# Optimization experiments

Hardware: AMD Instinct MI355X
Metric: run time of the kernel (lower is better)

The kernel has to match this reference:

```python
import jax, jax.numpy as jnp
import numpy as np

OUT_C, IN_C, K = 64, 64, 3
H, W = 32, 32


def setup_inputs() -> dict:
    key = jax.random.key(0)
    k1, k2, k3 = jax.random.split(key, 3)
    x = jax.random.normal(k1, (1, H, W, IN_C), dtype=jnp.float32)
    # One rational activation (P5/Q4, PAU 'version A') per (out_c, in_c, ky, kx)
    w_num = jax.random.normal(k2, (OUT_C, IN_C, K, K, 6), dtype=jnp.float32) * 0.1
    w_den = jax.random.normal(k3, (OUT_C, IN_C, K, K, 4), dtype=jnp.float32) * 0.1
    return {"x": x, "w_num": w_num, "w_den": w_den}


def reference(x, w_num, w_den):
    # x: [1, H, W, C] -- original module only supports batch=1 (squeeze semantics)
    h, w, c = x.shape[1], x.shape[2], x.shape[3]
    pad = (K - 1) // 2
    xp = jnp.pad(x[0], ((pad, pad), (pad, pad), (0, 0)))  # [H+2p, W+2p, C]
    # patches[a,b,i,j,c] = xp[i+a, j+b, c]  (same 'same-padding' sliding window)
    patches = jnp.stack(
        [jnp.stack([xp[a:a + h, b:b + w, :] for b in range(K)], axis=0)
         for a in range(K)], axis=0)  # [K,K,H,W,C]
    # powers x^0..x^5, computed once and reused by numerator and denominator
    pows = jnp.stack([patches ** n for n in range(6)], axis=0)  # [6,K,K,H,W,C]
    # per (f,c,a,b) rational: P(x) = sum_n a_n x^n,  Q(x) = 1 + |sum_{n=1..4} b_n x^n|
    P = jnp.einsum('nabijc,fcabn->fabijc', pows, w_num)
    Q = 1.0 + jnp.abs(jnp.einsum('nabijc,fcabn->fabijc', pows[1:5], w_den))
    # sum contributions over kernel positions (a,b) and input channels c
    return jnp.sum(P / Q, axis=(1, 2, 5))  # [OUT_C, H, W]
```

## Files before the change

kernel.cpp:

```cpp
#include <hip/hip_runtime.h>
#include <math.h>

#define NOUT 64
#define NIN  64
#define HH   32
#define WW   32

#define NREC      (NOUT * 9 * NIN)
#define WPK_ELEMS (NREC * 12)
#define WN_WORDS  (NOUT * NIN * 9 * 6)
#define WD_WORDS  (NOUT * NIN * 9 * 4)

__global__ __launch_bounds__(256) void wpack_kernel(const float* __restrict__ wn,
                                                    const float* __restrict__ wd,
                                                    float* __restrict__ wpk) {
    int idx = blockIdx.x * 256 + threadIdx.x;
    if (idx < WN_WORDS) {
        int n  = idx % 6;
        int t  = idx / 6;
        int ab = t % 9;
        int t2 = t / 9;
        int c  = t2 & 63;
        int f  = t2 >> 6;
        wpk[((f * 9 + ab) * 64 + c) * 12 + n] = wn[idx];
    } else {
        int id2 = idx - WN_WORDS;
        int n  = id2 & 3;
        int t  = id2 >> 2;
        int ab = t % 9;
        int t2 = t / 9;
        int c  = t2 & 63;
        int f  = t2 >> 6;
        wpk[((f * 9 + ab) * 64 + c) * 12 + 6 + n] = wd[id2];
    }
}

__global__ __launch_bounds__(512, 8) void kan_main(const float* __restrict__ x,
                                                   const float* __restrict__ wpk,
                                                   float* __restrict__ out) {
    __shared__ float xt[4 * 34 * 64];

    int bid  = blockIdx.x;
    int wgid = (bid & 7) * 128 + (bid >> 3);
    int f    = wgid >> 4;
    int band = wgid & 15;
    int i0   = band * 2;

    int tid  = threadIdx.x;
    int lane = tid & 63;
    int wave = tid >> 6;

#pragma unroll
    for (int k = 0; k < 17; ++k) {
        int idx = k * 512 + tid;
        int c   = idx & 63;
        int pos = idx >> 6;
        int col = pos % 34;
        int t   = pos / 34;
        int gi  = i0 - 1 + t;
        int gj  = col - 1;
        float v = 0.0f;
        if (gi >= 0 && gi < HH && gj >= 0 && gj < WW)
            v = x[(gi * WW + gj) * NIN + c];
        xt[idx] = v;
    }
    __syncthreads();

    int wr = wave >> 2;
    int j0 = (wave & 3) * 8;
    int i  = i0 + wr;

    float acc[8];
#pragma unroll
    for (int p = 0; p < 8; ++p) acc[p] = 0.0f;

    const float4* w4 = (const float4*)(wpk + ((size_t)(f * 9) * 64 + lane) * 12);

#pragma unroll 2
    for (int ab = 0; ab < 9; ++ab) {
        const int a = ab / 3, b = ab % 3;
        float4 wA = w4[ab * 192 + 0];
        float4 wB = w4[ab * 192 + 1];
        float4 wC = w4[ab * 192 + 2];

        const float* xb = &xt[((wr + a) * 34 + (j0 + b)) * 64 + lane];
#pragma unroll
        for (int p = 0; p < 8; ++p) {
            float xv = xb[p * 64];
            float pn = fmaf(wB.y, xv, wB.x);
            pn = fmaf(pn, xv, wA.w);
            pn = fmaf(pn, xv, wA.z);
            pn = fmaf(pn, xv, wA.y);
            pn = fmaf(pn, xv, wA.x);
            float qn = fmaf(wC.y, xv, wC.x);
            qn = fmaf(qn, xv, wB.w);
            qn = fmaf(qn, xv, wB.z);
            float den = 1.0f + fabsf(xv * qn);
            acc[p] = fmaf(pn, __builtin_amdgcn_rcpf(den), acc[p]);
        }
    }

#pragma unroll
    for (int p = 0; p < 8; ++p) {
        float s = acc[p];
        s += __shfl_xor(s, 32, 64);
        s += __shfl_xor(s, 16, 64);
        s += __shfl_xor(s, 8, 64);
        s += __shfl_xor(s, 4, 64);
        s += __shfl_xor(s, 2, 64);
        s += __shfl_xor(s, 1, 64);
        if (lane == p) out[f * (HH * WW) + i * WW + j0 + p] = s;
    }
}

__global__ __launch_bounds__(256) void kan_fallback(const float* __restrict__ x,
                                                    const float* __restrict__ wn,
                                                    const float* __restrict__ wd,
                                                    float* __restrict__ out) {
    __shared__ float red[256];
    int bid = blockIdx.x;
    int t = bid & 15;
    int f = bid >> 4;
    int tid = threadIdx.x;
    int g = tid >> 6;
    int p = tid & 63;
    int r = p >> 5;
    int j = p & 31;
    int i = t * 2 + r;
    int c0 = g * 16;
    const float* wnb = wn + (f * NIN + c0) * 9 * 6;
    const float* wdb = wd + (f * NIN + c0) * 9 * 4;
    float acc = 0.0f;
    for (int c = 0; c < 16; ++c) {
        float xv[9];
#pragma unroll
        for (int a = 0; a < 3; ++a)
#pragma unroll
            for (int b = 0; b < 3; ++b) {
                int ii = i + a - 1, jj = j + b - 1;
                bool inb = (ii >= 0) && (ii < HH) && (jj >= 0) && (jj < WW);
                xv[a * 3 + b] = inb ? x[(ii * WW + jj) * NIN + (c0 + c)] : 0.0f;
            }
        const float* wnc = wnb + c * 54;
        const float* wdc = wdb + c * 36;
#pragma unroll
        for (int ab = 0; ab < 9; ++ab) {
            float xx = xv[ab];
            float pn = fmaf(wnc[ab * 6 + 5], xx, wnc[ab * 6 + 4]);
            pn = fmaf(pn, xx, wnc[ab * 6 + 3]);
            pn = fmaf(pn, xx, wnc[ab * 6 + 2]);
            pn = fmaf(pn, xx, wnc[ab * 6 + 1]);
            pn = fmaf(pn, xx, wnc[ab * 6 + 0]);
            float qn = fmaf(wdc[ab * 4 + 3], xx, wdc[ab * 4 + 2]);
            qn = fmaf(qn, xx, wdc[ab * 4 + 1]);
            qn = fmaf(qn, xx, wdc[ab * 4 + 0]);
            float den = 1.0f + fabsf(xx * qn);
            acc = fmaf(pn, __builtin_amdgcn_rcpf(den), acc);
        }
    }
    red[tid] = acc;
    __syncthreads();
    if (tid < 64) {
        float s = red[tid] + red[tid + 64] + red[tid + 128] + red[tid + 192];
        int rr = tid >> 5;
        int jj = tid & 31;
        out[f * (HH * WW) + (t * 2 + rr) * WW + jj] = s;
    }
}

extern "C" void kernel_launch(void* const* d_in, const int* in_sizes, int n_in,
                              void* d_out, int out_size, void* d_ws, size_t ws_size,
                              hipStream_t stream) {
    const float* x  = (const float*)d_in[0];
    const float* wn = (const float*)d_in[1];
    const float* wd = (const float*)d_in[2];
    float* out = (float*)d_out;

    const size_t need = (size_t)WPK_ELEMS * sizeof(float);

    if (ws_size >= need) {
        float* wpk = (float*)d_ws;
        const int pack_total = WN_WORDS + WD_WORDS;
        wpack_kernel<<<pack_total / 256, 256, 0, stream>>>(wn, wd, wpk);
        kan_main<<<1024, 512, 0, stream>>>(x, wpk, out);
    } else {
        kan_fallback<<<NOUT * 16, 256, 0, stream>>>(x, wn, wd, out);
    }
}
```

Before: 28.08 us.

## Drop weight-pack kernel and remap threads to pixels with wave-uniform scalar weights

Removes the separate weight repacking launch and reads the original weight tensors directly. Each wave now owns 8 input channels and each lane one output pixel, so the weights are uniform across the wave (readfirstlane) and can be fetched with scalar loads. The input tile is transposed into a channel-major shared layout with an odd stride to avoid bank conflicts. The cross-lane shuffle reduction is replaced by an 8-way shared-memory reduction over waves. This saves one launch and the per-lane vector weight loads, at the cost of strided global-to-shared writes and a block barrier for the final reduction.

```diff
diff --git a/kernel.cpp b/kernel.cpp
--- a/kernel.cpp
+++ b/kernel.cpp
@@ -5,40 +5,14 @@
 #define NIN  64
 #define HH   32
 #define WW   32
-
-#define NREC      (NOUT * 9 * NIN)
-#define WPK_ELEMS (NREC * 12)
-#define WN_WORDS  (NOUT * NIN * 9 * 6)
-#define WD_WORDS  (NOUT * NIN * 9 * 4)
-
-__global__ __launch_bounds__(256) void wpack_kernel(const float* __restrict__ wn,
-                                                    const float* __restrict__ wd,
-                                                    float* __restrict__ wpk) {
-    int idx = blockIdx.x * 256 + threadIdx.x;
-    if (idx < WN_WORDS) {
-        int n  = idx % 6;
-        int t  = idx / 6;
-        int ab = t % 9;
-        int t2 = t / 9;
-        int c  = t2 & 63;
-        int f  = t2 >> 6;
-        wpk[((f * 9 + ab) * 64 + c) * 12 + n] = wn[idx];
-    } else {
-        int id2 = idx - WN_WORDS;
-        int n  = id2 & 3;
-        int t  = id2 >> 2;
-        int ab = t % 9;
-        int t2 = t / 9;
-        int c  = t2 & 63;
-        int f  = t2 >> 6;
-        wpk[((f * 9 + ab) * 64 + c) * 12 + 6 + n] = wd[id2];
-    }
-}
+#define XSTR 137
 
 __global__ __launch_bounds__(512, 8) void kan_main(const float* __restrict__ x,
-                                                   const float* __restrict__ wpk,
+                                                   const float* __restrict__ wn,
+                                                   const float* __restrict__ wd,
                                                    float* __restrict__ out) {
-    __shared__ float xt[4 * 34 * 64];
+    __shared__ float xt[NIN * XSTR];
+    __shared__ float red[512];
 
     int bid  = blockIdx.x;
     int wgid = (bid & 7) * 128 + (bid >> 3);
@@ -46,125 +20,66 @@
     int band = wgid & 15;
     int i0   = band * 2;
 
-    int tid  = threadIdx.x;
-    int lane = tid & 63;
-    int wave = tid >> 6;
+    int tid = threadIdx.x;
 
 #pragma unroll
     for (int k = 0; k < 17; ++k) {
         int idx = k * 512 + tid;
         int c   = idx & 63;
         int pos = idx >> 6;
+        int t   = pos / 34;
         int col = pos % 34;
-        int t   = pos / 34;
         int gi  = i0 - 1 + t;
         int gj  = col - 1;
         float v = 0.0f;
         if (gi >= 0 && gi < HH && gj >= 0 && gj < WW)
             v = x[(gi * WW + gj) * NIN + c];
-        xt[idx] = v;
+        xt[c * XSTR + pos] = v;
     }
     __syncthreads();
 
-    int wr = wave >> 2;
-    int j0 = (wave & 3) * 8;
-    int i  = i0 + wr;
+    int lane = tid & 63;
+    int wv   = __builtin_amdgcn_readfirstlane(tid >> 6);
+    int r    = lane >> 5;
+    int j    = lane & 31;
 
-    float acc[8];
+    float acc = 0.0f;
+
+    const float* wnf = wn + (size_t)(f * NIN + wv * 8) * 54;
+    const float* wdf = wd + (size_t)(f * NIN + wv * 8) * 36;
+
+    for (int cc = 0; cc < 8; ++cc) {
+        const float* wnc = wnf + cc * 54;
+        const float* wdc = wdf + cc * 36;
+        const float* xc  = &xt[(wv * 8 + cc) * XSTR + r * 34 + j];
 #pragma unroll
-    for (int p = 0; p < 8; ++p) acc[p] = 0.0f;
-
-    const float4* w4 = (const float4*)(wpk + ((size_t)(f * 9) * 64 + lane) * 12);
-
-#pragma unroll 2
-    for (int ab = 0; ab < 9; ++ab) {
-        const int a = ab / 3, b = ab % 3;
-        float4 wA = w4[ab * 192 + 0];
-        float4 wB = w4[ab * 192 + 1];
-        float4 wC = w4[ab * 192 + 2];
-
-        const float* xb = &xt[((wr + a) * 34 + (j0 + b)) * 64 + lane];
+        for (int a = 0; a < 3; ++a) {
 #pragma unroll
-        for (int p = 0; p < 8; ++p) {
-            float xv = xb[p * 64];
-            float pn = fmaf(wB.y, xv, wB.x);
-            pn = fmaf(pn, xv, wA.w);
-            pn = fmaf(pn, xv, wA.z);
-            pn = fmaf(pn, xv, wA.y);
-            pn = fmaf(pn, xv, wA.x);
-            float qn = fmaf(wC.y, xv, wC.x);
-            qn = fmaf(qn, xv, wB.w);
-            qn = fmaf(qn, xv, wB.z);
-            float den = 1.0f + fabsf(xv * qn);
-            acc[p] = fmaf(pn, __builtin_amdgcn_rcpf(den), acc[p]);
+            for (int b = 0; b < 3; ++b) {
+                const int ab = a * 3 + b;
+                float xv = xc[a * 34 + b];
+                float pn = fmaf(wnc[ab * 6 + 5], xv, wnc[ab * 6 + 4]);
+                pn = fmaf(pn, xv, wnc[ab * 6 + 3]);
+                pn = fmaf(pn, xv, wnc[ab * 6 + 2]);
+                pn = fmaf(pn, xv, wnc[ab * 6 + 1]);
+                pn = fmaf(pn, xv, wnc[ab * 6 + 0]);
+                float qn = fmaf(wdc[ab * 4 + 3], xv, wdc[ab * 4 + 2]);
+                qn = fmaf(qn, xv, wdc[ab * 4 + 1]);
+                qn = fmaf(qn, xv, wdc[ab * 4 + 0]);
+                float den = 1.0f + fabsf(xv * qn);
+                acc = fmaf(pn, __builtin_amdgcn_rcpf(den), acc);
+            }
         }
     }
 
-#pragma unroll
-    for (int p = 0; p < 8; ++p) {
-        float s = acc[p];
-        s += __shfl_xor(s, 32, 64);
-        s += __shfl_xor(s, 16, 64);
-        s += __shfl_xor(s, 8, 64);
-        s += __shfl_xor(s, 4, 64);
-        s += __shfl_xor(s, 2, 64);
-        s += __shfl_xor(s, 1, 64);
-        if (lane == p) out[f * (HH * WW) + i * WW + j0 + p] = s;
-    }
-}
-
-__global__ __launch_bounds__(256) void kan_fallback(const float* __restrict__ x,
-                                                    const float* __restrict__ wn,
-                                                    const float* __restrict__ wd,
-                                                    float* __restrict__ out) {
-    __shared__ float red[256];
-    int bid = blockIdx.x;
-    int t = bid & 15;
-    int f = bid >> 4;
-    int tid = threadIdx.x;
-    int g = tid >> 6;
-    int p = tid & 63;
-    int r = p >> 5;
-    int j = p & 31;
-    int i = t * 2 + r;
-    int c0 = g * 16;
-    const float* wnb = wn + (f * NIN + c0) * 9 * 6;
-    const float* wdb = wd + (f * NIN + c0) * 9 * 4;
-    float acc = 0.0f;
-    for (int c = 0; c < 16; ++c) {
-        float xv[9];
-#pragma unroll
-        for (int a = 0; a < 3; ++a)
-#pragma unroll
-            for (int b = 0; b < 3; ++b) {
-                int ii = i + a - 1, jj = j + b - 1;
-                bool inb = (ii >= 0) && (ii < HH) && (jj >= 0) && (jj < WW);
-                xv[a * 3 + b] = inb ? x[(ii * WW + jj) * NIN + (c0 + c)] : 0.0f;
-            }
-        const float* wnc = wnb + c * 54;
-        const float* wdc = wdb + c * 36;
-#pragma unroll
-        for (int ab = 0; ab < 9; ++ab) {
-            float xx = xv[ab];
-            float pn = fmaf(wnc[ab * 6 + 5], xx, wnc[ab * 6 + 4]);
-            pn = fmaf(pn, xx, wnc[ab * 6 + 3]);
-            pn = fmaf(pn, xx, wnc[ab * 6 + 2]);
-            pn = fmaf(pn, xx, wnc[ab * 6 + 1]);
-            pn = fmaf(pn, xx, wnc[ab * 6 + 0]);
-            float qn = fmaf(wdc[ab * 4 + 3], xx, wdc[ab * 4 + 2]);
-            qn = fmaf(qn, xx, wdc[ab * 4 + 1]);
-            qn = fmaf(qn, xx, wdc[ab * 4 + 0]);
-            float den = 1.0f + fabsf(xx * qn);
-            acc = fmaf(pn, __builtin_amdgcn_rcpf(den), acc);
-        }
-    }
     red[tid] = acc;
     __syncthreads();
     if (tid < 64) {
-        float s = red[tid] + red[tid + 64] + red[tid + 128] + red[tid + 192];
+        float s = red[tid]       + red[tid + 64]  + red[tid + 128] + red[tid + 192]
+                + red[tid + 256] + red[tid + 320] + red[tid + 384] + red[tid + 448];
         int rr = tid >> 5;
         int jj = tid & 31;
-        out[f * (HH * WW) + (t * 2 + rr) * WW + jj] = s;
+        out[f * (HH * WW) + (i0 + rr) * WW + jj] = s;
     }
 }
 
@@ -175,15 +90,7 @@
     const float* wn = (const float*)d_in[1];
     const float* wd = (const float*)d_in[2];
     float* out = (float*)d_out;
+    (void)d_ws; (void)ws_size;
 
-    const size_t need = (size_t)WPK_ELEMS * sizeof(float);
-
-    if (ws_size >= need) {
-        float* wpk = (float*)d_ws;
-        const int pack_total = WN_WORDS + WD_WORDS;
-        wpack_kernel<<<pack_total / 256, 256, 0, stream>>>(wn, wd, wpk);
-        kan_main<<<1024, 512, 0, stream>>>(x, wpk, out);
-    } else {
-        kan_fallback<<<NOUT * 16, 256, 0, stream>>>(x, wn, wd, out);
-    }
+    kan_main<<<1024, 512, 0, stream>>>(x, wn, wd, out);
 }
```

New measurement: 23.59 us. 1.19x faster.
